# Performance work log

Measured on AMD Instinct MI355X. Metric: run time of the kernel, lower is better.

Reference implementation:

```python
import jax, jax.numpy as jnp
import numpy as np

N = 50000
IN_DIM = 512
OUT_DIM = 128
E = 800000
EPS = 1e-5


def setup_inputs() -> dict:
    key = jax.random.key(0)
    ks = jax.random.split(key, 12)
    x = jax.random.normal(ks[0], (N, IN_DIM), dtype=jnp.float32)
    edge_index = jax.random.randint(ks[1], (2, E), 0, N, dtype=jnp.int64)
    s1 = 1.0 / np.sqrt(IN_DIM)
    s2 = 1.0 / np.sqrt(OUT_DIM)
    W1 = jax.random.normal(ks[2], (IN_DIM, OUT_DIM), dtype=jnp.float32) * s1
    b1 = jnp.zeros((OUT_DIM,), jnp.float32)
    W2 = jax.random.normal(ks[3], (OUT_DIM, OUT_DIM), dtype=jnp.float32) * s2
    b2 = jnp.zeros((OUT_DIM,), jnp.float32)
    W3 = jax.random.normal(ks[4], (OUT_DIM, OUT_DIM), dtype=jnp.float32) * s2
    b3 = jnp.zeros((OUT_DIM,), jnp.float32)
    g1 = jnp.ones((OUT_DIM,), jnp.float32)
    be1 = jnp.zeros((OUT_DIM,), jnp.float32)
    g2 = jnp.ones((OUT_DIM,), jnp.float32)
    be2 = jnp.zeros((OUT_DIM,), jnp.float32)
    a1 = jnp.full((1,), 0.25, jnp.float32)  # PReLU weight
    a2 = jnp.full((1,), 0.25, jnp.float32)
    return {"x": x, "edge_index": edge_index, "W1": W1, "b1": b1, "W2": W2,
            "b2": b2, "W3": W3, "b3": b3, "g1": g1, "be1": be1, "g2": g2,
            "be2": be2, "a1": a1, "a2": a2}


def _gcn_norm(edge_index, n):
    # add self-loops, symmetric normalization deg^-1/2 A deg^-1/2
    loop = jnp.arange(n, dtype=edge_index.dtype)
    src = jnp.concatenate([edge_index[0], loop])
    dst = jnp.concatenate([edge_index[1], loop])
    deg = jax.ops.segment_sum(jnp.ones_like(dst, jnp.float32), dst, num_segments=n)
    dinv = jax.lax.rsqrt(jnp.maximum(deg, 1.0))
    norm = dinv[src] * dinv[dst]
    return src, dst, norm


def _gcn_conv(x, W, b, src, dst, norm, n):
    h = x @ W                                   # [N, out]
    msg = h[src] * norm[:, None]                # gather + scale over edges
    agg = jax.ops.segment_sum(msg, dst, num_segments=n)
    return agg + b


def _bn(x, g, b):
    mean = jnp.mean(x, axis=0)
    var = jnp.var(x, axis=0)  # biased, as torch BN uses for normalization
    return (x - mean) * jax.lax.rsqrt(var + EPS) * g + b


def _prelu(x, a):
    return jnp.where(x >= 0, x, a * x)


def reference(x, edge_index, W1, b1, W2, b2, W3, b3, g1, be1, g2, be2, a1, a2):
    src, dst, norm = _gcn_norm(edge_index, N)
    h = _gcn_conv(x, W1, b1, src, dst, norm, N)
    h = _prelu(_bn(h, g1, be1), a1)
    h = _gcn_conv(h, W2, b2, src, dst, norm, N)
    h = _prelu(_bn(h, g2, be2), a2)
    h = _gcn_conv(h, W3, b3, src, dst, norm, N)
    return h
```

## Files before the change

### kernel.cpp

```cpp
#include <hip/hip_runtime.h>

#define N_NODES 50000
#define IN_DIM  512
#define OUT_DIM 128
#define BN_EPS  1e-5f

typedef __attribute__((ext_vector_type(8))) short short8;
typedef __attribute__((ext_vector_type(4))) float f32x4;

__device__ __forceinline__ unsigned short bf16_rne(float x) {
    unsigned u = __float_as_uint(x);
    unsigned r = (u + 0x7FFFu + ((u >> 16) & 1u)) >> 16;
    return (unsigned short)r;
}
__device__ __forceinline__ float bf16_to_f(unsigned short s) {
    return __uint_as_float(((unsigned)s) << 16);
}

__device__ __forceinline__ void gload16(const void* g, void* l) {
    __builtin_amdgcn_global_load_lds(
        (const __attribute__((address_space(1))) void*)g,
        (__attribute__((address_space(3))) void*)l, 16, 0, 0);
}


__device__ __forceinline__ int edge_is64(const int* ei) {
    return (ei[1] | ei[3] | ei[5] | ei[7]) == 0;
}

__global__ __launch_bounds__(256) void deg_wconv(
        const int* __restrict__ ei, int* __restrict__ cnt, int E,
        const float* __restrict__ W1, short* __restrict__ Wt1,
        const float* __restrict__ W2, short* __restrict__ Wt2,
        const float* __restrict__ W3, short* __restrict__ Wt3) {
    const int degBlocks = (E + 255) / 256;
    const int b = blockIdx.x;
    __shared__ short tile[64][130];
    if (b < degBlocks) {
        int e = b * 256 + threadIdx.x;
        if (e >= E) return;
        int dst;
        if (edge_is64(ei)) dst = ((const int2*)ei)[E + e].x;
        else               dst = ei[E + e];
        atomicAdd(&cnt[dst], 1);
    } else {
        const int wb = b - degBlocks;
        const float* W; short* Wt; int K, k0;
        if (wb < 8)       { W = W1; Wt = Wt1; K = IN_DIM;  k0 = wb * 64; }
        else if (wb < 10) { W = W2; Wt = Wt2; K = OUT_DIM; k0 = (wb - 8) * 64; }
        else              { W = W3; Wt = Wt3; K = OUT_DIM; k0 = (wb - 10) * 64; }
        for (int i = threadIdx.x; i < 64 * 128; i += 256) {
            int k = i >> 7, c = i & 127;
            tile[k][c] = (short)bf16_rne(W[(size_t)(k0 + k) * 128 + c]);
        }
        __syncthreads();
        for (int i = threadIdx.x; i < 64 * 128; i += 256) {
            int c = i >> 6, k = i & 63;
            Wt[(size_t)c * K + k0 + k] = tile[k][c];
        }
    }
}


__global__ __launch_bounds__(1024) void scan_partial(const int* __restrict__ cnt,
                                                     int* __restrict__ psum, int n) {
    __shared__ int wsum[16];
    const int i = blockIdx.x * 1024 + threadIdx.x;
    const int lane = threadIdx.x & 63;
    const int wv = threadIdx.x >> 6;
    int v = (i < n) ? cnt[i] + 1 : 0;
#pragma unroll
    for (int d = 1; d < 64; d <<= 1) v += __shfl_xor(v, d);
    if (lane == 0) wsum[wv] = v;
    __syncthreads();
    if (threadIdx.x == 0) {
        int t = 0;
#pragma unroll
        for (int w = 0; w < 16; ++w) t += wsum[w];
        psum[blockIdx.x] = t;
    }
}

__global__ void scan_base(const int* __restrict__ psum, int* __restrict__ pbase,
                          int* __restrict__ rowp, int nb, int n) {
    const int lane = threadIdx.x;
    int orig = (lane < nb) ? psum[lane] : 0;
    int v = orig;
#pragma unroll
    for (int d = 1; d < 64; d <<= 1) {
        int t = __shfl_up(v, d);
        if (lane >= d) v += t;
    }
    if (lane < nb) pbase[lane] = v - orig;
    if (lane == nb - 1) rowp[n] = v;
}

__global__ __launch_bounds__(1024) void scan_final(int* __restrict__ cnt,
                                                   const int* __restrict__ pbase,
                                                   int* __restrict__ rowp,
                                                   float* __restrict__ dinv,
                                                   unsigned short* __restrict__ col, int n) {
    __shared__ int wsum[16];
    const int i = blockIdx.x * 1024 + threadIdx.x;
    const int lane = threadIdx.x & 63;
    const int wv = threadIdx.x >> 6;
    int orig = (i < n) ? cnt[i] + 1 : 0;
    int v = orig;
#pragma unroll
    for (int d = 1; d < 64; d <<= 1) {
        int t = __shfl_up(v, d);
        if (lane >= d) v += t;
    }
    if (lane == 63) wsum[wv] = v;
    __syncthreads();
    int woff = 0;
    for (int w = 0; w < wv; ++w) woff += wsum[w];
    if (i < n) {
        int rp = pbase[blockIdx.x] + woff + v - orig;
        rowp[i] = rp;
        dinv[i] = rsqrtf(fmaxf((float)orig, 1.f));
        col[rp] = (unsigned short)i;
        cnt[i] = rp + 1;
    }
}


template <typename TA, int K, bool XFORM>
__device__ __forceinline__ void gemm_body(
        int bid, const TA* __restrict__ A, const short* __restrict__ Wt,
        unsigned short* __restrict__ out, int M,
        const float* __restrict__ stats, const float* __restrict__ gam,
        const float* __restrict__ bet, const float* __restrict__ alpha_p,
        const float* __restrict__ dinv) {
    constexpr int BK = 64;
    constexpr int NSTEP = K / BK;
    constexpr int UPRA = (BK * (int)sizeof(TA)) / 16;
    constexpr int AINST = 64 * UPRA / 256;
    __shared__ TA    ldsA[64 * BK];
    __shared__ short ldsB[128 * BK];
    __shared__ float bnp[256];

    const int tid  = threadIdx.x;
    const int lane = tid & 63;
    const int wv   = tid >> 6;
    const int r16  = lane & 15;
    const int g    = lane >> 4;
    const int row0 = bid * 64;
    const int arow_t = wv * 16 + r16;

    float alpha = 0.f;
    if constexpr (XFORM) {
        alpha = alpha_p[0];
        if (tid < 128) {
            float sum = 0.f, sq = 0.f;
#pragma unroll
            for (int r = 0; r < 8; ++r) {
                sum += stats[r * 256 + tid];
                sq  += stats[r * 256 + 128 + tid];
            }
            const float inv_n = 1.0f / (float)N_NODES;
            float mean = sum * inv_n;
            float var = fmaxf(sq * inv_n - mean * mean, 0.f);
            float sc = gam[tid] * rsqrtf(var + BN_EPS);
            bnp[tid] = sc;
            bnp[128 + tid] = bet[tid] - mean * sc;
        }
        __syncthreads();
    }

    f32x4 acc[8];
#pragma unroll
    for (int nf = 0; nf < 8; nf++) acc[nf] = (f32x4)(0.f);

    for (int s = 0; s < NSTEP; ++s) {
        const int k0 = s * BK;
        if (s) __syncthreads();
#pragma unroll
        for (int i = 0; i < AINST; ++i) {
            const int d   = i * 256 + tid;
            const int row = d / UPRA, p = d % UPRA;
            int grow = row0 + row; if (grow >= M) grow = M - 1;
            const char* src = (const char*)(A + (size_t)grow * K + k0) + ((p ^ (row & 7)) * 16);
            gload16(src, (char*)ldsA + (size_t)(i * 256 + wv * 64) * 16);
        }
#pragma unroll
        for (int i = 0; i < 4; ++i) {
            const int d    = i * 256 + tid;
            const int colb = d >> 3, p = d & 7;
            const short* src = Wt + (size_t)colb * K + k0 + (p ^ (colb & 7)) * 8;
            gload16(src, (char*)ldsB + (size_t)(i * 256 + wv * 64) * 16);
        }
        __syncthreads();
#pragma unroll
        for (int ksub = 0; ksub < 2; ++ksub) {
            short8 af;
            if constexpr (sizeof(TA) == 4) {
                const int q0 = ksub * 8 + g * 2;
                const float4* A4 = (const float4*)ldsA;
                float4 alo = A4[arow_t * UPRA + (q0 ^ (r16 & 7))];
                float4 ahi = A4[arow_t * UPRA + ((q0 + 1) ^ (r16 & 7))];
                float av[8] = {alo.x, alo.y, alo.z, alo.w, ahi.x, ahi.y, ahi.z, ahi.w};
#pragma unroll
                for (int j = 0; j < 8; j++) af[j] = (short)bf16_rne(av[j]);
            } else {
                short8 raw = ((const short8*)ldsA)[arow_t * 8 + ((ksub * 4 + g) ^ (r16 & 7))];
                if constexpr (XFORM) {
                    const int kb = k0 + ksub * 32 + g * 8;
#pragma unroll
                    for (int j = 0; j < 8; j++) {
                        float v = fmaf(bf16_to_f((unsigned short)raw[j]), bnp[kb + j], bnp[128 + kb + j]);
                        v = v >= 0.f ? v : alpha * v;
                        af[j] = (short)bf16_rne(v);
                    }
                } else {
                    af = raw;
                }
            }
#pragma unroll
            for (int nf = 0; nf < 8; nf++) {
                const int colb = nf * 16 + r16;
                short8 bf = ((const short8*)ldsB)[colb * 8 + ((ksub * 4 + g) ^ (r16 & 7))];
                acc[nf] = __builtin_amdgcn_mfma_f32_16x16x32_bf16(af, bf, acc[nf], 0, 0, 0);
            }
        }
    }

    __syncthreads();
    unsigned short* ot = (unsigned short*)ldsB;
#pragma unroll
    for (int r = 0; r < 4; ++r) {
        const int trow = wv * 16 + g * 4 + r;
        const int grow = row0 + trow;
        const float dv = (grow < M) ? dinv[grow] : 0.f;
#pragma unroll
        for (int nf = 0; nf < 8; nf++)
            ot[trow * 128 + nf * 16 + r16] = bf16_rne(acc[nf][r] * dv);
    }
    __syncthreads();
    {
        const int trow = wv * 16 + r16;
        const int seg  = g;
        const int grow = row0 + trow;
        if (grow < M) {
            const float4* lsrc = (const float4*)ot + trow * 16 + seg * 4;
            float4* gdst = (float4*)((char*)out + (size_t)grow * 256) + seg * 4;
#pragma unroll
            for (int i = 0; i < 4; ++i) gdst[i] = lsrc[i];
        }
    }
}


__global__ __launch_bounds__(256) void gemm1_fill(
        const float* __restrict__ A, const short* __restrict__ Wt,
        unsigned short* __restrict__ out, int M, const float* __restrict__ dinv,
        const int* __restrict__ ei, int* __restrict__ cnt,
        unsigned short* __restrict__ col, int E, int gblocks) {
    if ((int)blockIdx.x < gblocks) {
        gemm_body<float, IN_DIM, false>(blockIdx.x, A, Wt, out, M,
                                        nullptr, nullptr, nullptr, nullptr, dinv);
    } else {
        int e = (blockIdx.x - gblocks) * 256 + threadIdx.x;
        if (e >= E) return;
        int src, dst;
        if (edge_is64(ei)) { src = ((const int2*)ei)[e].x; dst = ((const int2*)ei)[E + e].x; }
        else               { src = ei[e];                  dst = ei[E + e]; }
        int pos = atomicAdd(&cnt[dst], 1);
        col[pos] = (unsigned short)src;
    }
}

template <typename TA, int K, bool XFORM>
__global__ __launch_bounds__(256) void mfma_gemm(
        const TA* __restrict__ A, const short* __restrict__ Wt,
        unsigned short* __restrict__ out, int M,
        const float* __restrict__ stats, const float* __restrict__ gam,
        const float* __restrict__ bet, const float* __restrict__ alpha_p,
        const float* __restrict__ dinv) {
    gemm_body<TA, K, XFORM>(blockIdx.x, A, Wt, out, M, stats, gam, bet, alpha_p, dinv);
}


template <int FINAL>
__global__ __launch_bounds__(256) void agg_kernel(
        const unsigned short* __restrict__ h, const int* __restrict__ rowp,
        const unsigned short* __restrict__ col, const float* __restrict__ dinv,
        const float* __restrict__ bias, void* __restrict__ outv,
        float* __restrict__ stats, int n) {
    const int wave = threadIdx.x >> 6;
    const int lane = threadIdx.x & 63;
    const int f = lane << 1;
    const float b0 = bias[f], b1 = bias[f + 1];
    float s0 = 0.f, s1 = 0.f, q0 = 0.f, q1 = 0.f;
    const int stride = gridDim.x << 2;
    for (int node = (blockIdx.x << 2) + wave; node < n; node += stride) {
        int e = rowp[node];
        const int end = rowp[node + 1];
        float a0 = 0.f, a1 = 0.f;
        for (; e + 8 <= end; e += 8) {
            int c[8];
#pragma unroll
            for (int j = 0; j < 8; j++) c[j] = col[e + j];
            unsigned v[8];
#pragma unroll
            for (int j = 0; j < 8; j++) v[j] = *(const unsigned*)(h + (size_t)c[j] * OUT_DIM + f);
#pragma unroll
            for (int j = 0; j < 8; j++) {
                a0 += __uint_as_float(v[j] << 16);
                a1 += __uint_as_float(v[j] & 0xFFFF0000u);
            }
        }
        for (; e < end; ++e) {
            unsigned v = *(const unsigned*)(h + (size_t)col[e] * OUT_DIM + f);
            a0 += __uint_as_float(v << 16);
            a1 += __uint_as_float(v & 0xFFFF0000u);
        }
        float dn = dinv[node];
        a0 = fmaf(a0, dn, b0);
        a1 = fmaf(a1, dn, b1);
        if (FINAL) {
            ((float2*)outv)[(size_t)node * 64 + lane] = make_float2(a0, a1);
        } else {
            unsigned p = ((unsigned)bf16_rne(a1) << 16) | (unsigned)bf16_rne(a0);
            ((unsigned*)outv)[(size_t)node * 64 + lane] = p;
            s0 += a0; s1 += a1;
            q0 = fmaf(a0, a0, q0); q1 = fmaf(a1, a1, q1);
        }
    }
    if (!FINAL) {
        __shared__ float red[4][256];
        red[wave][f] = s0;        red[wave][f + 1] = s1;
        red[wave][128 + f] = q0;  red[wave][128 + f + 1] = q1;
        __syncthreads();
        int t = threadIdx.x;
        float v = red[0][t] + red[1][t] + red[2][t] + red[3][t];
        atomicAdd(&stats[(blockIdx.x & 7) * 256 + t], v);
    }
}


extern "C" void kernel_launch(void* const* d_in, const int* in_sizes, int n_in,
                              void* d_out, int out_size, void* d_ws, size_t ws_size,
                              hipStream_t stream) {
    const float* x   = (const float*)d_in[0];
    const int*   ei  = (const int*)d_in[1];
    const float* W1  = (const float*)d_in[2];
    const float* b1  = (const float*)d_in[3];
    const float* W2  = (const float*)d_in[4];
    const float* b2  = (const float*)d_in[5];
    const float* W3  = (const float*)d_in[6];
    const float* b3  = (const float*)d_in[7];
    const float* g1  = (const float*)d_in[8];
    const float* be1 = (const float*)d_in[9];
    const float* g2  = (const float*)d_in[10];
    const float* be2 = (const float*)d_in[11];
    const float* a1  = (const float*)d_in[12];
    const float* a2  = (const float*)d_in[13];

    const int n = N_NODES;
    const int E = in_sizes[1] / 2;
    float* out = (float*)d_out;

    char* ws = (char*)d_ws;
    size_t off = 0;
    auto alloc = [&](size_t bytes) { void* p = ws + off; off += (bytes + 255) & ~(size_t)255; return p; };
    unsigned short* bufA = (unsigned short*)alloc((size_t)n * OUT_DIM * sizeof(short));
    unsigned short* hb   = (unsigned short*)alloc((size_t)n * OUT_DIM * sizeof(short));
    size_t zero_beg = off;
    int*   cnt   = (int*)alloc((size_t)n * sizeof(int));
    float* stats = (float*)alloc(4096 * sizeof(float));
    size_t zero_end = off;
    int*   rowp  = (int*)alloc((size_t)(n + 1) * sizeof(int));
    float* dinv  = (float*)alloc((size_t)n * sizeof(float));
    unsigned short* col = (unsigned short*)alloc((size_t)(E + n) * sizeof(unsigned short));
    short* Wt1   = (short*)alloc((size_t)IN_DIM * OUT_DIM * sizeof(short));
    short* Wt2   = (short*)alloc((size_t)OUT_DIM * OUT_DIM * sizeof(short));
    short* Wt3   = (short*)alloc((size_t)OUT_DIM * OUT_DIM * sizeof(short));
    int*   psum  = (int*)alloc(64 * sizeof(int));
    int*   pbase = (int*)alloc(64 * sizeof(int));

    const int nbScan = (n + 1023) / 1024;
    const int degBlocks = (E + 255) / 256;
    const int gblocks = (n + 63) / 64;
    const int ablocks = 2048;

    hipMemsetAsync(ws + zero_beg, 0, zero_end - zero_beg, stream);
    hipLaunchKernelGGL(deg_wconv, dim3(degBlocks + 12), dim3(256), 0, stream,
                       ei, cnt, E, W1, Wt1, W2, Wt2, W3, Wt3);
    hipLaunchKernelGGL(scan_partial, dim3(nbScan), dim3(1024), 0, stream, cnt, psum, n);
    hipLaunchKernelGGL(scan_base, dim3(1), dim3(64), 0, stream, psum, pbase, rowp, nbScan, n);
    hipLaunchKernelGGL(scan_final, dim3(nbScan), dim3(1024), 0, stream, cnt, pbase, rowp, dinv, col, n);

    hipLaunchKernelGGL(gemm1_fill, dim3(gblocks + degBlocks), dim3(256), 0, stream,
                       x, Wt1, bufA, n, dinv, ei, cnt, col, E, gblocks);
    hipLaunchKernelGGL((agg_kernel<0>), dim3(ablocks), dim3(256), 0, stream,
                       bufA, rowp, col, dinv, b1, hb, stats, n);
    hipLaunchKernelGGL((mfma_gemm<short, OUT_DIM, true>), dim3(gblocks), dim3(256), 0, stream,
                       (const short*)hb, Wt2, bufA, n, stats, g1, be1, a1, dinv);
    hipLaunchKernelGGL((agg_kernel<0>), dim3(ablocks), dim3(256), 0, stream,
                       bufA, rowp, col, dinv, b2, hb, stats + 2048, n);
    hipLaunchKernelGGL((mfma_gemm<short, OUT_DIM, true>), dim3(gblocks), dim3(256), 0, stream,
                       (const short*)hb, Wt3, bufA, n, stats + 2048, g2, be2, a2, dinv);
    hipLaunchKernelGGL((agg_kernel<1>), dim3(ablocks), dim3(256), 0, stream,
                       bufA, rowp, col, dinv, b3, out, nullptr, n);
}
```

Before: 272.7 us.

## Partition degree and CSR-fill atomics by destination range per XCD

```diff
diff --git a/kernel.cpp b/kernel.cpp
--- a/kernel.cpp
+++ b/kernel.cpp
@@ -4,6 +4,7 @@
 #define IN_DIM  512
 #define OUT_DIM 128
 #define BN_EPS  1e-5f
+#define NODES_PER_XCD 6250
 
 typedef __attribute__((ext_vector_type(8))) short short8;
 typedef __attribute__((ext_vector_type(4))) float f32x4;
@@ -33,16 +34,22 @@
         const float* __restrict__ W1, short* __restrict__ Wt1,
         const float* __restrict__ W2, short* __restrict__ Wt2,
         const float* __restrict__ W3, short* __restrict__ Wt3) {
-    const int degBlocks = (E + 255) / 256;
+    const int degBlocks = 8 * ((E + 2047) / 2048);
     const int b = blockIdx.x;
     __shared__ short tile[64][130];
     if (b < degBlocks) {
-        int e = b * 256 + threadIdx.x;
-        if (e >= E) return;
-        int dst;
-        if (edge_is64(ei)) dst = ((const int2*)ei)[E + e].x;
-        else               dst = ei[E + e];
-        atomicAdd(&cnt[dst], 1);
+        const int lo = (b & 7) * NODES_PER_XCD;
+        const int hi = lo + NODES_PER_XCD;
+        const int base = (b >> 3) * 2048;
+        const int is64 = edge_is64(ei);
+#pragma unroll
+        for (int j = 0; j < 8; ++j) {
+            int e = base + j * 256 + threadIdx.x;
+            if (e < E) {
+                int dst = is64 ? ((const int2*)ei)[E + e].x : ei[E + e];
+                if (dst >= lo && dst < hi) atomicAdd(&cnt[dst], 1);
+            }
+        }
     } else {
         const int wb = b - degBlocks;
         const float* W; short* Wt; int K, k0;
@@ -260,13 +267,24 @@
         gemm_body<float, IN_DIM, false>(blockIdx.x, A, Wt, out, M,
                                         nullptr, nullptr, nullptr, nullptr, dinv);
     } else {
-        int e = (blockIdx.x - gblocks) * 256 + threadIdx.x;
-        if (e >= E) return;
-        int src, dst;
-        if (edge_is64(ei)) { src = ((const int2*)ei)[e].x; dst = ((const int2*)ei)[E + e].x; }
-        else               { src = ei[e];                  dst = ei[E + e]; }
-        int pos = atomicAdd(&cnt[dst], 1);
-        col[pos] = (unsigned short)src;
+        const int fb = blockIdx.x - gblocks;
+        const int lo = (fb & 7) * NODES_PER_XCD;
+        const int hi = lo + NODES_PER_XCD;
+        const int base = (fb >> 3) * 2048;
+        const int is64 = edge_is64(ei);
+#pragma unroll
+        for (int j = 0; j < 8; ++j) {
+            int e = base + j * 256 + threadIdx.x;
+            if (e < E) {
+                int src, dst;
+                if (is64) { src = ((const int2*)ei)[e].x; dst = ((const int2*)ei)[E + e].x; }
+                else      { src = ei[e];                  dst = ei[E + e]; }
+                if (dst >= lo && dst < hi) {
+                    int pos = atomicAdd(&cnt[dst], 1);
+                    col[pos] = (unsigned short)src;
+                }
+            }
+        }
     }
 }
 
@@ -380,18 +398,18 @@
     int*   pbase = (int*)alloc(64 * sizeof(int));
 
     const int nbScan = (n + 1023) / 1024;
-    const int degBlocks = (E + 255) / 256;
+    const int partBlocks = 8 * ((E + 2047) / 2048);
     const int gblocks = (n + 63) / 64;
     const int ablocks = 2048;
 
     hipMemsetAsync(ws + zero_beg, 0, zero_end - zero_beg, stream);
-    hipLaunchKernelGGL(deg_wconv, dim3(degBlocks + 12), dim3(256), 0, stream,
+    hipLaunchKernelGGL(deg_wconv, dim3(partBlocks + 12), dim3(256), 0, stream,
                        ei, cnt, E, W1, Wt1, W2, Wt2, W3, Wt3);
     hipLaunchKernelGGL(scan_partial, dim3(nbScan), dim3(1024), 0, stream, cnt, psum, n);
     hipLaunchKernelGGL(scan_base, dim3(1), dim3(64), 0, stream, psum, pbase, rowp, nbScan, n);
     hipLaunchKernelGGL(scan_final, dim3(nbScan), dim3(1024), 0, stream, cnt, pbase, rowp, dinv, col, n);
 
-    hipLaunchKernelGGL(gemm1_fill, dim3(gblocks + degBlocks), dim3(256), 0, stream,
+    hipLaunchKernelGGL(gemm1_fill, dim3(gblocks + partBlocks), dim3(256), 0, stream,
                        x, Wt1, bufA, n, dinv, ei, cnt, col, E, gblocks);
     hipLaunchKernelGGL((agg_kernel<0>), dim3(ablocks), dim3(256), 0, stream,
                        bufA, rowp, col, dinv, b1, hb, stats, n);
```

Result: faster. 257.8 us (-5.5%).
